# Kernel optimization log

Measured on AMD Instinct MI355X. Metric: run time of the kernel, lower is better.

Reference implementation:

```python
import jax, jax.numpy as jnp
import numpy as np


def setup_inputs() -> dict:
    key = jax.random.key(0)
    kq, kk, kv, kl = jax.random.split(key, 4)
    B, Nq, Nk, D, Dv = 16, 2048, 2048, 128, 128
    queries = jax.random.normal(kq, (B, Nq, D), dtype=jnp.float32)
    keys = jax.random.normal(kk, (B, Nk, D), dtype=jnp.float32)
    values = jax.random.normal(kv, (B, Nk, Dv), dtype=jnp.float32)
    valid_lens = jax.random.randint(kl, (B,), 0, 2048, dtype=jnp.int64)
    return {"queries": queries, "keys": keys, "values": values, "valid_lens": valid_lens}


def reference(queries, keys, values, valid_lens):
    # queries: (B, Nq, d), keys: (B, Nk, d), values: (B, Nk, dv), valid_lens: (B,)
    d = queries.shape[-1]
    scores = jnp.einsum('bqd,bkd->bqk', queries, keys) / jnp.sqrt(jnp.asarray(d, queries.dtype))
    # masked_softmax: original sets masked score positions to 1e-8 (NOT -inf) before softmax
    nk = scores.shape[-1]
    mask = jnp.arange(nk)[None, :] < valid_lens[:, None]  # (B, Nk)
    scores = jnp.where(mask[:, None, :], scores, jnp.asarray(1e-8, scores.dtype))
    attn = jax.nn.softmax(scores, axis=-1)
    # dropout rate 0.0 -> identity (eval semantics)
    return jnp.einsum('bqk,bkv->bqv', attn, values)
```

## Files before the change

### kernel.cpp

```cpp
#include <hip/hip_runtime.h>
#include <stdint.h>

#define BATCH 16
#define NQ    2048
#define NK    2048
#define DD    128
#define DVV   128

typedef __bf16 bf16_t;
typedef __bf16 bf16x2 __attribute__((ext_vector_type(2)));
typedef __bf16 bf16x4 __attribute__((ext_vector_type(4)));
typedef __bf16 bf16x8 __attribute__((ext_vector_type(8)));
typedef float  f32x4  __attribute__((ext_vector_type(4)));

#define KB_OFF   ((size_t)0)
#define VT_OFF   ((size_t)8 * 1024 * 1024)
#define SUF_OFF  ((size_t)16 * 1024 * 1024)
#define SCH_OFF  (SUF_OFF + 65536)
#define WS_NEED  (SCH_OFF + 4096)

__device__ __forceinline__ int load_valid_len(const int* VL, int b) {
  bool looks64 = true;
#pragma unroll
  for (int i = 0; i < 16; ++i) {
    int hi = VL[2 * i + 1];
    unsigned lo = (unsigned)VL[2 * i];
    looks64 = looks64 && (hi == 0) && (lo <= 2048u);
  }
  int L = looks64 ? VL[2 * b] : VL[b];
  return min(max(L, 0), NK);
}

__device__ __forceinline__ void gld16(const void* g, void* l) {
  __builtin_amdgcn_global_load_lds(
      (const __attribute__((address_space(1))) unsigned int*)g,
      (__attribute__((address_space(3))) unsigned int*)l, 16, 0, 0);
}

__device__ __forceinline__ f32x4 mfma16(bf16x8 a, bf16x8 b, f32x4 c) {
  return __builtin_amdgcn_mfma_f32_16x16x32_bf16(a, b, c, 0, 0, 0);
}

__global__ void prep_kernel(const float* __restrict__ K, const float* __restrict__ V,
                            const int* __restrict__ VL,
                            bf16_t* __restrict__ Kb, bf16_t* __restrict__ Vt,
                            float* __restrict__ sufV, int* __restrict__ sched) {
  __shared__ bf16_t tile2[64 * 136];
  __shared__ float sred[16 * 128];
  __shared__ int bs[16];
  const int bid = blockIdx.x;
  const int t = threadIdx.x;
  if (bid < 512) {
#pragma unroll
    for (int i = 0; i < 4; ++i) {
      size_t f4 = (size_t)bid * 2048 + (size_t)i * 512 + 2 * t;
      float4 a = ((const float4*)K)[f4];
      float4 c = ((const float4*)K)[f4 + 1];
      bf16x8 o;
      o[0] = (bf16_t)a.x; o[1] = (bf16_t)a.y; o[2] = (bf16_t)a.z; o[3] = (bf16_t)a.w;
      o[4] = (bf16_t)c.x; o[5] = (bf16_t)c.y; o[6] = (bf16_t)c.z; o[7] = (bf16_t)c.w;
      ((bf16x8*)Kb)[f4 >> 1] = o;
    }
    return;
  }
  if (bid < 1024) {
    int v = bid - 512;
    int b = v & 15, kt = v >> 4;
    int L = load_valid_len(VL, b);
    const bool anymask = (kt * 64 + 64 > L);

    float sacc[8];
#pragma unroll
    for (int j = 0; j < 8; ++j) sacc[j] = 0.f;
    const int c0 = (t & 15) * 8;
#pragma unroll
    for (int i = 0; i < 4; ++i) {
      int rl = i * 16 + (t >> 4);
      const float* src = V + ((size_t)b * NK + kt * 64 + rl) * DVV + c0;
      float4 u0 = ((const float4*)src)[0];
      float4 u1 = ((const float4*)src)[1];
      bf16x8 o;
      o[0] = (bf16_t)u0.x; o[1] = (bf16_t)u0.y; o[2] = (bf16_t)u0.z; o[3] = (bf16_t)u0.w;
      o[4] = (bf16_t)u1.x; o[5] = (bf16_t)u1.y; o[6] = (bf16_t)u1.z; o[7] = (bf16_t)u1.w;
      *(bf16x8*)&tile2[rl * 136 + c0] = o;
      if (kt * 64 + rl >= L) {
        sacc[0] += u0.x; sacc[1] += u0.y; sacc[2] += u0.z; sacc[3] += u0.w;
        sacc[4] += u1.x; sacc[5] += u1.y; sacc[6] += u1.z; sacc[7] += u1.w;
      }
    }
    __syncthreads();

    if (anymask) {
#pragma unroll
      for (int j = 0; j < 8; ++j) sred[(t >> 4) * 128 + c0 + j] = sacc[j];
      __syncthreads();
      if (t < 128) {
        float s = 0.f;
#pragma unroll
        for (int g = 0; g < 16; ++g) s += sred[g * 128 + t];
        atomicAdd(&sufV[b * 128 + t], s);
      }
    }

    int dv = t >> 1, half = t & 1;
    bf16_t* dst = Vt + (size_t)b * DVV * NK + (size_t)dv * NK + kt * 64 + half * 32;
#pragma unroll
    for (int jj = 0; jj < 4; ++jj) {
      bf16x8 o;
#pragma unroll
      for (int k8 = 0; k8 < 8; ++k8)
        o[k8] = tile2[(half * 32 + jj * 8 + k8) * 136 + dv];
      *(bf16x8*)(dst + jj * 8) = o;
    }
    return;
  }
  if (t == 0) {
    int Ls[16], idx[16];
#pragma unroll
    for (int i = 0; i < 16; ++i) { Ls[i] = load_valid_len(VL, i); idx[i] = i; }
    for (int i = 1; i < 16; ++i) {
      int lv = Ls[i], iv = idx[i], j = i - 1;
      while (j >= 0 && Ls[j] < lv) { Ls[j + 1] = Ls[j]; idx[j + 1] = idx[j]; --j; }
      Ls[j + 1] = lv; idx[j + 1] = iv;
    }
#pragma unroll
    for (int i = 0; i < 16; ++i) bs[i] = idx[i];
  }
  __syncthreads();
  for (int j = t; j < 512; j += 256) {
    int r = (j < 256) ? j : (767 - j);
    sched[j] = (bs[r >> 5] << 5) | (r & 31);
  }
}

__launch_bounds__(256, 2)
__global__ void attn_kernel(const float* __restrict__ Q, const bf16_t* __restrict__ Kb,
                            const bf16_t* __restrict__ Vt, const int* __restrict__ VL,
                            const float* __restrict__ sufV, const int* __restrict__ sched,
                            float* __restrict__ Out) {
  __shared__ __align__(16) char smem[73984];
  bf16_t* sK = (bf16_t*)smem;
  bf16_t* sV = (bf16_t*)(smem + 32768);

  const int unit = sched[blockIdx.x];
  const int b  = (unit >> 5) & 15;
  const int qt = unit & 31;
  const int L  = load_valid_len(VL, b);
  const int ktiles = (L + 63) >> 6;

  const int tid = threadIdx.x;
  const int wave = tid >> 6;
  const int lane = tid & 63;
  const int col = lane & 15;
  const int quad = lane >> 4;
  const int wr = wave >> 1;
  const int wc = wave & 1;

  bf16_t* pw = (bf16_t*)(smem + 65536 + wave * 2048);

  bf16x8 qf[2][4];
  {
    const float scq = 0.1275174307f;
#pragma unroll
    for (int m = 0; m < 2; ++m) {
      const float* qrow = Q + ((size_t)b * NQ + qt * 64 + wr * 32 + m * 16 + col) * DD + quad * 8;
#pragma unroll
      for (int ks = 0; ks < 4; ++ks) {
        float4 u0 = *(const float4*)(qrow + ks * 32);
        float4 u1 = *(const float4*)(qrow + ks * 32 + 4);
        bf16x8 f;
        f[0] = (bf16_t)(u0.x * scq); f[1] = (bf16_t)(u0.y * scq);
        f[2] = (bf16_t)(u0.z * scq); f[3] = (bf16_t)(u0.w * scq);
        f[4] = (bf16_t)(u1.x * scq); f[5] = (bf16_t)(u1.y * scq);
        f[6] = (bf16_t)(u1.z * scq); f[7] = (bf16_t)(u1.w * scq);
        qf[m][ks] = f;
      }
    }
  }

  const char* Kbyte = (const char*)Kb + (size_t)b * NK * DD * 2;
  const char* Vbyte = (const char*)Vt + (size_t)b * DVV * NK * 2;
  int koff[4], voff[4];
#pragma unroll
  for (int i = 0; i < 4; ++i) {
    int krow = wave * 16 + i * 4 + (lane >> 4);
    koff[i] = krow * 256 + (((lane & 15) ^ (krow & 15)) * 16);
    int vrow = wave * 32 + i * 8 + (lane >> 3);
    voff[i] = vrow * (NK * 2) + (((lane & 7) ^ ((lane >> 3) & 7)) * 16);
  }

  f32x4 Oacc[2][8];
#pragma unroll
  for (int m = 0; m < 2; ++m)
#pragma unroll
    for (int o = 0; o < 8; ++o) Oacc[m][o] = (f32x4){0.f, 0.f, 0.f, 0.f};
  float lsum[2] = {0.f, 0.f};

  auto issueTile = [&](int kt, int bufi) {
    const char* kb = Kbyte + (size_t)kt * 16384;
    const char* vb = Vbyte + (size_t)kt * 128;
    bf16_t* kl = sK + bufi * 8192 + wave * 2048;
    bf16_t* vl = sV + bufi * 8192 + wave * 2048;
#pragma unroll
    for (int i = 0; i < 4; ++i) {
      gld16(kb + koff[i], kl + i * 512);
      gld16(vb + voff[i], vl + i * 512);
    }
  };

  if (ktiles > 0) issueTile(0, 0);
  int bufi = 0;
  for (int kt = 0; kt < ktiles; ++kt) {
    asm volatile("s_waitcnt vmcnt(0)\n\ts_barrier" ::: "memory");
    if (kt + 1 < ktiles) issueTile(kt + 1, bufi ^ 1);

    const bf16_t* kb_ = sK + bufi * 8192;
    const bf16_t* vb_ = sV + bufi * 8192;

    f32x4 sc[2][2];
#pragma unroll
    for (int ntk = 0; ntk < 2; ++ntk)
#pragma unroll
      for (int m = 0; m < 2; ++m) sc[ntk][m] = (f32x4){0.f, 0.f, 0.f, 0.f};
    __builtin_amdgcn_s_setprio(1);
#pragma unroll
    for (int ks = 0; ks < 4; ++ks) {
#pragma unroll
      for (int ntk = 0; ntk < 2; ++ntk) {
        bf16x8 kf = *(const bf16x8*)&kb_[(wc * 32 + ntk * 16 + col) * 128 + (((ks * 4 + quad) ^ col) * 8)];
        sc[ntk][0] = mfma16(kf, qf[0][ks], sc[ntk][0]);
        sc[ntk][1] = mfma16(kf, qf[1][ks], sc[ntk][1]);
      }
    }
    __builtin_amdgcn_s_setprio(0);

    const int kbase = kt * 64 + wc * 32;
#pragma unroll
    for (int ntk = 0; ntk < 2; ++ntk) {
#pragma unroll
      for (int m = 0; m < 2; ++m) {
        float pv[4];
#pragma unroll
        for (int r = 0; r < 4; ++r) {
          float p = __builtin_amdgcn_exp2f(sc[ntk][m][r]);
          p = (kbase + ntk * 16 + quad * 4 + r < L) ? p : 0.f;
          lsum[m] += p;
          pv[r] = p;
        }
        int cidx = m * 4 + ntk * 2 + (quad >> 1);
        int phys = cidx ^ (col & 7);
        *(bf16x4*)&pw[col * 64 + phys * 8 + (quad & 1) * 4] =
            (bf16x4){(bf16_t)pv[0], (bf16_t)pv[1], (bf16_t)pv[2], (bf16_t)pv[3]};
      }
    }

    bf16x8 pa[2];
#pragma unroll
    for (int m = 0; m < 2; ++m)
      pa[m] = *(const bf16x8*)&pw[col * 64 + (((m * 4 + quad) ^ (col & 7)) * 8)];
    __builtin_amdgcn_s_setprio(1);
#pragma unroll
    for (int o = 0; o < 8; ++o) {
      bf16x8 bb = *(const bf16x8*)&vb_[(o * 16 + col) * 64 + (((wc * 4 + quad) ^ (col & 7)) * 8)];
      Oacc[0][o] = mfma16(pa[0], bb, Oacc[0][o]);
      Oacc[1][o] = mfma16(pa[1], bb, Oacc[1][o]);
    }
    __builtin_amdgcn_s_setprio(0);
    bufi ^= 1;
  }
  __syncthreads();

#pragma unroll
  for (int m = 0; m < 2; ++m) {
    lsum[m] += __shfl_xor(lsum[m], 16, 64);
    lsum[m] += __shfl_xor(lsum[m], 32, 64);
  }

  float* scrO = (float*)(smem + wr * 18432);
  float* scrL = (float*)(smem + 73728) + wr * 32;

  if (wc == 1) {
#pragma unroll
    for (int m = 0; m < 2; ++m)
#pragma unroll
      for (int o = 0; o < 8; ++o)
        *(f32x4*)&scrO[(o * 16 + col) * 36 + m * 16 + quad * 4] = Oacc[m][o];
    if (quad == 0) {
#pragma unroll
      for (int m = 0; m < 2; ++m) scrL[m * 16 + col] = lsum[m];
    }
  }
  __syncthreads();
  if (wc == 0) {
    const float wmask = (float)(NK - L);
    float inv[2];
#pragma unroll
    for (int m = 0; m < 2; ++m)
      inv[m] = 1.0f / (lsum[m] + scrL[m * 16 + col] + wmask);
    float invq[2][4];
#pragma unroll
    for (int m = 0; m < 2; ++m)
#pragma unroll
      for (int r = 0; r < 4; ++r)
        invq[m][r] = __shfl(inv[m], quad * 4 + r, 64);
    const float* sfv = sufV + b * DVV;
    float* Ob = Out + ((size_t)b * NQ + qt * 64 + wr * 32) * DVV;
#pragma unroll
    for (int m = 0; m < 2; ++m)
#pragma unroll
      for (int o = 0; o < 8; ++o) {
        f32x4 part = *(const f32x4*)&scrO[(o * 16 + col) * 36 + m * 16 + quad * 4];
        float svv = sfv[o * 16 + col];
#pragma unroll
        for (int r = 0; r < 4; ++r)
          Ob[(size_t)(m * 16 + quad * 4 + r) * DVV + o * 16 + col] =
              (Oacc[m][o][r] + part[r] + svv) * invq[m][r];
      }
  }
}

#define KSTR 152
#define VSTR 88
#define PSTR 72

__global__ void suffix_fb(const float* __restrict__ V, const int* __restrict__ VL,
                          float* __restrict__ ws) {
  int b = blockIdx.x;
  int kc = blockIdx.y;
  int L = load_valid_len(VL, b);
  int k0 = kc * 128, k1 = k0 + 128;
  int lo = max(L, k0);
  int t = threadIdx.x;
  int dv = t & 127;
  int h = t >> 7;
  float s = 0.f;
  for (int k = lo + h; k < k1; k += 2)
    s += V[((size_t)b * NK + k) * DVV + dv];
  __shared__ float part[128];
  if (h == 0) part[dv] = s;
  __syncthreads();
  if (h == 1) atomicAdd(&ws[b * DVV + dv], part[dv] + s);
}

__launch_bounds__(256, 2)
__global__ void attn_fb(const float* __restrict__ Q, const float* __restrict__ K,
                        const float* __restrict__ V, const int* __restrict__ VL,
                        const float* __restrict__ sufV, float* __restrict__ Out) {
  const int flat = blockIdx.x;
  const int b  = flat & 15;
  const int qt = flat >> 4;
  const int L  = load_valid_len(VL, b);

  __shared__ bf16_t sK2[64 * KSTR];
  __shared__ bf16_t sVT2[128 * VSTR];
  __shared__ bf16_t sP2[4 * 16 * PSTR];

  const int tid  = threadIdx.x;
  const int wave = tid >> 6;
  const int lane = tid & 63;
  const int col  = lane & 15;
  const int quad = lane >> 4;

  const float* Qb = Q + ((size_t)b * NQ + qt * 64 + wave * 16) * DD;
  const float* Kb = K + (size_t)b * NK * DD;
  const float* Vb = V + (size_t)b * NK * DVV;

  bf16x8 qf[4];
  {
    const float scq = 0.08838834764831845f;
    const float* qrow = Qb + (size_t)col * DD + quad * 8;
#pragma unroll
    for (int ks = 0; ks < 4; ++ks) {
      float4 u0 = *(const float4*)(qrow + ks * 32);
      float4 u1 = *(const float4*)(qrow + ks * 32 + 4);
      bf16x8 f;
      f[0] = (bf16_t)(u0.x * scq); f[1] = (bf16_t)(u0.y * scq);
      f[2] = (bf16_t)(u0.z * scq); f[3] = (bf16_t)(u0.w * scq);
      f[4] = (bf16_t)(u1.x * scq); f[5] = (bf16_t)(u1.y * scq);
      f[6] = (bf16_t)(u1.z * scq); f[7] = (bf16_t)(u1.w * scq);
      qf[ks] = f;
    }
  }

  f32x4 Oacc[8];
#pragma unroll
  for (int o = 0; o < 8; ++o) Oacc[o] = (f32x4){0.f, 0.f, 0.f, 0.f};
  float m_i[4], l_i[4];
#pragma unroll
  for (int r = 0; r < 4; ++r) { m_i[r] = -1e30f; l_i[r] = 0.f; }

  const int ktiles = (L + 63) >> 6;
  for (int kt = 0; kt < ktiles; ++kt) {
    {
      int r0 = tid >> 5;
      int d4 = (tid & 31) * 4;
      const float* src = Kb + ((size_t)(kt * 64) + r0) * DD + d4;
#pragma unroll
      for (int i = 0; i < 8; ++i) {
        float4 u = *(const float4*)(src + (size_t)i * 8 * DD);
        bf16x4 w4 = {(bf16_t)u.x, (bf16_t)u.y, (bf16_t)u.z, (bf16_t)u.w};
        *(bf16x4*)&sK2[(r0 + i * 8) * KSTR + d4] = w4;
      }
    }
    {
      int r2 = (tid & 31) * 2;
      int dbase = (tid >> 5) * 4;
#pragma unroll
      for (int i = 0; i < 4; ++i) {
        int d4 = dbase + i * 32;
        const float* s0 = Vb + ((size_t)(kt * 64) + r2) * DVV + d4;
        float4 u0 = *(const float4*)s0;
        float4 u1 = *(const float4*)(s0 + DVV);
        *(bf16x2*)&sVT2[(d4 + 0) * VSTR + r2] = (bf16x2){(bf16_t)u0.x, (bf16_t)u1.x};
        *(bf16x2*)&sVT2[(d4 + 1) * VSTR + r2] = (bf16x2){(bf16_t)u0.y, (bf16_t)u1.y};
        *(bf16x2*)&sVT2[(d4 + 2) * VSTR + r2] = (bf16x2){(bf16_t)u0.z, (bf16_t)u1.z};
        *(bf16x2*)&sVT2[(d4 + 3) * VSTR + r2] = (bf16x2){(bf16_t)u0.w, (bf16_t)u1.w};
      }
    }
    __syncthreads();

    f32x4 sv4[4];
#pragma unroll
    for (int nt = 0; nt < 4; ++nt) sv4[nt] = (f32x4){0.f, 0.f, 0.f, 0.f};
#pragma unroll
    for (int ks = 0; ks < 4; ++ks) {
      bf16x8 a = qf[ks];
#pragma unroll
      for (int nt = 0; nt < 4; ++nt) {
        bf16x8 bb = *(const bf16x8*)&sK2[(nt * 16 + col) * KSTR + ks * 32 + quad * 8];
        sv4[nt] = mfma16(a, bb, sv4[nt]);
      }
    }

    const int key0 = kt * 64;
    float sv[4][4];
    float mloc[4] = {-1e30f, -1e30f, -1e30f, -1e30f};
#pragma unroll
    for (int nt = 0; nt < 4; ++nt) {
      int key = key0 + nt * 16 + col;
      bool valid = key < L;
#pragma unroll
      for (int r = 0; r < 4; ++r) {
        float v = valid ? sv4[nt][r] : -1e30f;
        sv[nt][r] = v;
        mloc[r] = fmaxf(mloc[r], v);
      }
    }
#pragma unroll
    for (int off = 1; off < 16; off <<= 1)
#pragma unroll
      for (int r = 0; r < 4; ++r) mloc[r] = fmaxf(mloc[r], __shfl_xor(mloc[r], off, 64));
    float al[4];
#pragma unroll
    for (int r = 0; r < 4; ++r) {
      float mn = fmaxf(m_i[r], mloc[r]);
      al[r] = __expf(m_i[r] - mn);
      m_i[r] = mn;
    }
    float lloc[4] = {0.f, 0.f, 0.f, 0.f};
#pragma unroll
    for (int nt = 0; nt < 4; ++nt)
#pragma unroll
      for (int r = 0; r < 4; ++r) {
        float p = __expf(sv[nt][r] - m_i[r]);
        sv[nt][r] = p;
        lloc[r] += p;
      }
#pragma unroll
    for (int off = 1; off < 16; off <<= 1)
#pragma unroll
      for (int r = 0; r < 4; ++r) lloc[r] += __shfl_xor(lloc[r], off, 64);
#pragma unroll
    for (int r = 0; r < 4; ++r) l_i[r] = l_i[r] * al[r] + lloc[r];
#pragma unroll
    for (int o = 0; o < 8; ++o)
#pragma unroll
      for (int r = 0; r < 4; ++r) Oacc[o][r] *= al[r];

    bf16_t* pw = &sP2[wave * 16 * PSTR];
#pragma unroll
    for (int nt = 0; nt < 4; ++nt)
#pragma unroll
      for (int r = 0; r < 4; ++r)
        pw[(quad * 4 + r) * PSTR + nt * 16 + col] = (bf16_t)sv[nt][r];

#pragma unroll
    for (int ks2 = 0; ks2 < 2; ++ks2) {
      bf16x8 a = *(const bf16x8*)&pw[(lane & 15) * PSTR + ks2 * 32 + quad * 8];
#pragma unroll
      for (int o = 0; o < 8; ++o) {
        bf16x8 bb = *(const bf16x8*)&sVT2[(o * 16 + col) * VSTR + ks2 * 32 + quad * 8];
        Oacc[o] = mfma16(a, bb, Oacc[o]);
      }
    }
    __syncthreads();
  }

  if (L < NK) {
    const float c = 1e-8f;
    const float w = (float)(NK - L);
    float a2[4], ec[4];
#pragma unroll
    for (int r = 0; r < 4; ++r) {
      float mn = fmaxf(m_i[r], c);
      a2[r] = __expf(m_i[r] - mn);
      ec[r] = __expf(c - mn);
      l_i[r] = l_i[r] * a2[r] + w * ec[r];
    }
    const float* sfv = sufV + b * DVV;
#pragma unroll
    for (int o = 0; o < 8; ++o) {
      float svv = sfv[o * 16 + col];
#pragma unroll
      for (int r = 0; r < 4; ++r) Oacc[o][r] = Oacc[o][r] * a2[r] + ec[r] * svv;
    }
  }

  float invl[4];
#pragma unroll
  for (int r = 0; r < 4; ++r) invl[r] = 1.0f / l_i[r];

  float* Ob = Out + ((size_t)b * NQ + qt * 64 + wave * 16) * DVV;
#pragma unroll
  for (int o = 0; o < 8; ++o)
#pragma unroll
    for (int r = 0; r < 4; ++r)
      Ob[(size_t)(quad * 4 + r) * DVV + o * 16 + col] = Oacc[o][r] * invl[r];
}

extern "C" void kernel_launch(void* const* d_in, const int* in_sizes, int n_in,
                              void* d_out, int out_size, void* d_ws, size_t ws_size,
                              hipStream_t stream) {
  const float* Q  = (const float*)d_in[0];
  const float* K  = (const float*)d_in[1];
  const float* V  = (const float*)d_in[2];
  const int*   VL = (const int*)d_in[3];
  float* out = (float*)d_out;

  if (ws_size >= WS_NEED) {
    char* ws = (char*)d_ws;
    bf16_t* Kb = (bf16_t*)(ws + KB_OFF);
    bf16_t* Vt = (bf16_t*)(ws + VT_OFF);
    float* sufV = (float*)(ws + SUF_OFF);
    int* sched = (int*)(ws + SCH_OFF);

    hipMemsetAsync(sufV, 0, BATCH * DVV * sizeof(float), stream);
    prep_kernel<<<1025, 256, 0, stream>>>(K, V, VL, Kb, Vt, sufV, sched);
    attn_kernel<<<512, 256, 0, stream>>>(Q, Kb, Vt, VL, sufV, sched, out);
  } else {
    float* ws = (float*)d_ws;
    hipMemsetAsync(ws, 0, BATCH * DVV * sizeof(float), stream);
    dim3 g1(BATCH, 16);
    suffix_fb<<<g1, 256, 0, stream>>>(V, VL, ws);
    attn_fb<<<BATCH * (NQ / 64), 256, 0, stream>>>(Q, K, V, VL, ws, out);
  }
}
```

Measured before the change: 141.9 us.

## Drop memset and schedule table; fuse K/V prep blocks, reduce suffix partials in attention

The hipMemsetAsync and the atomic suffix accumulation are removed. Each prep block now writes a per-tile partial masked-value sum, which the attention kernel reduces in its epilogue. The K-conversion and V-transpose blocks are merged into one 512-block prep kernel, and each attention block now computes the length-sorted schedule itself instead of reading a precomputed table. This saves a launch and the atomics, at the cost of a small redundant sort and 32 extra partial-sum loads per attention block.

```diff
diff --git a/kernel.cpp b/kernel.cpp
--- a/kernel.cpp
+++ b/kernel.cpp
@@ -15,9 +15,8 @@
 
 #define KB_OFF   ((size_t)0)
 #define VT_OFF   ((size_t)8 * 1024 * 1024)
-#define SUF_OFF  ((size_t)16 * 1024 * 1024)
-#define SCH_OFF  (SUF_OFF + 65536)
-#define WS_NEED  (SCH_OFF + 4096)
+#define PSUF_OFF ((size_t)16 * 1024 * 1024)
+#define WS_NEED  (PSUF_OFF + 262144)
 
 __device__ __forceinline__ int load_valid_len(const int* VL, int b) {
   bool looks64 = true;
@@ -41,114 +40,97 @@
   return __builtin_amdgcn_mfma_f32_16x16x32_bf16(a, b, c, 0, 0, 0);
 }
 
-__global__ void prep_kernel(const float* __restrict__ K, const float* __restrict__ V,
-                            const int* __restrict__ VL,
-                            bf16_t* __restrict__ Kb, bf16_t* __restrict__ Vt,
-                            float* __restrict__ sufV, int* __restrict__ sched) {
+__global__ void prep2_kernel(const float* __restrict__ Kf, const float* __restrict__ Vf,
+                             const int* __restrict__ VL,
+                             bf16_t* __restrict__ Kb, bf16_t* __restrict__ Vt,
+                             float* __restrict__ partSuf) {
   __shared__ bf16_t tile2[64 * 136];
   __shared__ float sred[16 * 128];
-  __shared__ int bs[16];
-  const int bid = blockIdx.x;
+  const int g = blockIdx.x;
   const int t = threadIdx.x;
-  if (bid < 512) {
-#pragma unroll
-    for (int i = 0; i < 4; ++i) {
-      size_t f4 = (size_t)bid * 2048 + (size_t)i * 512 + 2 * t;
-      float4 a = ((const float4*)K)[f4];
-      float4 c = ((const float4*)K)[f4 + 1];
-      bf16x8 o;
-      o[0] = (bf16_t)a.x; o[1] = (bf16_t)a.y; o[2] = (bf16_t)a.z; o[3] = (bf16_t)a.w;
-      o[4] = (bf16_t)c.x; o[5] = (bf16_t)c.y; o[6] = (bf16_t)c.z; o[7] = (bf16_t)c.w;
-      ((bf16x8*)Kb)[f4 >> 1] = o;
-    }
-    return;
-  }
-  if (bid < 1024) {
-    int v = bid - 512;
-    int b = v & 15, kt = v >> 4;
-    int L = load_valid_len(VL, b);
-    const bool anymask = (kt * 64 + 64 > L);
-
-    float sacc[8];
-#pragma unroll
-    for (int j = 0; j < 8; ++j) sacc[j] = 0.f;
-    const int c0 = (t & 15) * 8;
-#pragma unroll
-    for (int i = 0; i < 4; ++i) {
-      int rl = i * 16 + (t >> 4);
-      const float* src = V + ((size_t)b * NK + kt * 64 + rl) * DVV + c0;
-      float4 u0 = ((const float4*)src)[0];
-      float4 u1 = ((const float4*)src)[1];
-      bf16x8 o;
-      o[0] = (bf16_t)u0.x; o[1] = (bf16_t)u0.y; o[2] = (bf16_t)u0.z; o[3] = (bf16_t)u0.w;
-      o[4] = (bf16_t)u1.x; o[5] = (bf16_t)u1.y; o[6] = (bf16_t)u1.z; o[7] = (bf16_t)u1.w;
-      *(bf16x8*)&tile2[rl * 136 + c0] = o;
-      if (kt * 64 + rl >= L) {
-        sacc[0] += u0.x; sacc[1] += u0.y; sacc[2] += u0.z; sacc[3] += u0.w;
-        sacc[4] += u1.x; sacc[5] += u1.y; sacc[6] += u1.z; sacc[7] += u1.w;
-      }
-    }
-    __syncthreads();
-
-    if (anymask) {
-#pragma unroll
-      for (int j = 0; j < 8; ++j) sred[(t >> 4) * 128 + c0 + j] = sacc[j];
-      __syncthreads();
-      if (t < 128) {
-        float s = 0.f;
-#pragma unroll
-        for (int g = 0; g < 16; ++g) s += sred[g * 128 + t];
-        atomicAdd(&sufV[b * 128 + t], s);
-      }
-    }
-
-    int dv = t >> 1, half = t & 1;
-    bf16_t* dst = Vt + (size_t)b * DVV * NK + (size_t)dv * NK + kt * 64 + half * 32;
-#pragma unroll
-    for (int jj = 0; jj < 4; ++jj) {
-      bf16x8 o;
-#pragma unroll
-      for (int k8 = 0; k8 < 8; ++k8)
-        o[k8] = tile2[(half * 32 + jj * 8 + k8) * 136 + dv];
-      *(bf16x8*)(dst + jj * 8) = o;
-    }
-    return;
-  }
-  if (t == 0) {
-    int Ls[16], idx[16];
-#pragma unroll
-    for (int i = 0; i < 16; ++i) { Ls[i] = load_valid_len(VL, i); idx[i] = i; }
-    for (int i = 1; i < 16; ++i) {
-      int lv = Ls[i], iv = idx[i], j = i - 1;
-      while (j >= 0 && Ls[j] < lv) { Ls[j + 1] = Ls[j]; idx[j + 1] = idx[j]; --j; }
-      Ls[j + 1] = lv; idx[j + 1] = iv;
-    }
-#pragma unroll
-    for (int i = 0; i < 16; ++i) bs[i] = idx[i];
+
+#pragma unroll
+  for (int i = 0; i < 4; ++i) {
+    size_t f4 = (size_t)g * 2048 + (size_t)i * 512 + 2 * t;
+    float4 a = ((const float4*)Kf)[f4];
+    float4 c = ((const float4*)Kf)[f4 + 1];
+    bf16x8 o;
+    o[0] = (bf16_t)a.x; o[1] = (bf16_t)a.y; o[2] = (bf16_t)a.z; o[3] = (bf16_t)a.w;
+    o[4] = (bf16_t)c.x; o[5] = (bf16_t)c.y; o[6] = (bf16_t)c.z; o[7] = (bf16_t)c.w;
+    ((bf16x8*)Kb)[f4 >> 1] = o;
+  }
+
+  int b = g & 15, kt = g >> 4;
+  int L = load_valid_len(VL, b);
+  float sacc[8];
+#pragma unroll
+  for (int j = 0; j < 8; ++j) sacc[j] = 0.f;
+  const int c0 = (t & 15) * 8;
+#pragma unroll
+  for (int i = 0; i < 4; ++i) {
+    int rl = i * 16 + (t >> 4);
+    const float* src = Vf + ((size_t)b * NK + kt * 64 + rl) * DVV + c0;
+    float4 u0 = ((const float4*)src)[0];
+    float4 u1 = ((const float4*)src)[1];
+    bf16x8 o;
+    o[0] = (bf16_t)u0.x; o[1] = (bf16_t)u0.y; o[2] = (bf16_t)u0.z; o[3] = (bf16_t)u0.w;
+    o[4] = (bf16_t)u1.x; o[5] = (bf16_t)u1.y; o[6] = (bf16_t)u1.z; o[7] = (bf16_t)u1.w;
+    *(bf16x8*)&tile2[rl * 136 + c0] = o;
+    if (kt * 64 + rl >= L) {
+      sacc[0] += u0.x; sacc[1] += u0.y; sacc[2] += u0.z; sacc[3] += u0.w;
+      sacc[4] += u1.x; sacc[5] += u1.y; sacc[6] += u1.z; sacc[7] += u1.w;
+    }
   }
   __syncthreads();
-  for (int j = t; j < 512; j += 256) {
-    int r = (j < 256) ? j : (767 - j);
-    sched[j] = (bs[r >> 5] << 5) | (r & 31);
+#pragma unroll
+  for (int j = 0; j < 8; ++j) sred[(t >> 4) * 128 + c0 + j] = sacc[j];
+  __syncthreads();
+  if (t < 128) {
+    float s = 0.f;
+#pragma unroll
+    for (int gg = 0; gg < 16; ++gg) s += sred[gg * 128 + t];
+    partSuf[(size_t)g * 128 + t] = s;
+  }
+  int dv = t >> 1, half = t & 1;
+  bf16_t* dst = Vt + (size_t)b * DVV * NK + (size_t)dv * NK + kt * 64 + half * 32;
+#pragma unroll
+  for (int jj = 0; jj < 4; ++jj) {
+    bf16x8 o;
+#pragma unroll
+    for (int k8 = 0; k8 < 8; ++k8)
+      o[k8] = tile2[(half * 32 + jj * 8 + k8) * 136 + dv];
+    *(bf16x8*)(dst + jj * 8) = o;
   }
 }
 
 __launch_bounds__(256, 2)
 __global__ void attn_kernel(const float* __restrict__ Q, const bf16_t* __restrict__ Kb,
                             const bf16_t* __restrict__ Vt, const int* __restrict__ VL,
-                            const float* __restrict__ sufV, const int* __restrict__ sched,
-                            float* __restrict__ Out) {
+                            const float* __restrict__ partSuf, float* __restrict__ Out) {
   __shared__ __align__(16) char smem[73984];
   bf16_t* sK = (bf16_t*)smem;
   bf16_t* sV = (bf16_t*)(smem + 32768);
 
-  const int unit = sched[blockIdx.x];
+  const int tid = threadIdx.x;
+  int unit;
+  {
+    int Ls[16], idx[16];
+#pragma unroll
+    for (int i = 0; i < 16; ++i) { Ls[i] = load_valid_len(VL, i); idx[i] = i; }
+    for (int i = 1; i < 16; ++i) {
+      int lv = Ls[i], iv = idx[i], jj = i - 1;
+      while (jj >= 0 && Ls[jj] < lv) { Ls[jj + 1] = Ls[jj]; idx[jj + 1] = idx[jj]; --jj; }
+      Ls[jj + 1] = lv; idx[jj + 1] = iv;
+    }
+    int gg = blockIdx.x;
+    int r = (gg < 256) ? gg : (767 - gg);
+    unit = (idx[r >> 5] << 5) | (r & 31);
+  }
   const int b  = (unit >> 5) & 15;
   const int qt = unit & 31;
   const int L  = load_valid_len(VL, b);
   const int ktiles = (L + 63) >> 6;
 
-  const int tid = threadIdx.x;
   const int wave = tid >> 6;
   const int lane = tid & 63;
   const int col = lane & 15;
@@ -270,6 +252,16 @@
   }
   __syncthreads();
 
+  float* sred2 = (float*)(smem + 36864);
+  {
+    int dv = tid & 127, h = tid >> 7;
+    float part = 0.f;
+#pragma unroll
+    for (int j = 0; j < 16; ++j)
+      part += partSuf[(size_t)((h * 16 + j) * 16 + b) * 128 + dv];
+    sred2[tid] = part;
+  }
+
 #pragma unroll
   for (int m = 0; m < 2; ++m) {
     lsum[m] += __shfl_xor(lsum[m], 16, 64);
@@ -303,14 +295,13 @@
 #pragma unroll
       for (int r = 0; r < 4; ++r)
         invq[m][r] = __shfl(inv[m], quad * 4 + r, 64);
-    const float* sfv = sufV + b * DVV;
     float* Ob = Out + ((size_t)b * NQ + qt * 64 + wr * 32) * DVV;
 #pragma unroll
     for (int m = 0; m < 2; ++m)
 #pragma unroll
       for (int o = 0; o < 8; ++o) {
         f32x4 part = *(const f32x4*)&scrO[(o * 16 + col) * 36 + m * 16 + quad * 4];
-        float svv = sfv[o * 16 + col];
+        float svv = sred2[o * 16 + col] + sred2[128 + o * 16 + col];
 #pragma unroll
         for (int r = 0; r < 4; ++r)
           Ob[(size_t)(m * 16 + quad * 4 + r) * DVV + o * 16 + col] =
@@ -541,12 +532,10 @@
     char* ws = (char*)d_ws;
     bf16_t* Kb = (bf16_t*)(ws + KB_OFF);
     bf16_t* Vt = (bf16_t*)(ws + VT_OFF);
-    float* sufV = (float*)(ws + SUF_OFF);
-    int* sched = (int*)(ws + SCH_OFF);
-
-    hipMemsetAsync(sufV, 0, BATCH * DVV * sizeof(float), stream);
-    prep_kernel<<<1025, 256, 0, stream>>>(K, V, VL, Kb, Vt, sufV, sched);
-    attn_kernel<<<512, 256, 0, stream>>>(Q, Kb, Vt, VL, sufV, sched, out);
+    float* psuf = (float*)(ws + PSUF_OFF);
+
+    prep2_kernel<<<512, 256, 0, stream>>>(K, V, VL, Kb, Vt, psuf);
+    attn_kernel<<<512, 256, 0, stream>>>(Q, Kb, Vt, VL, psuf, out);
   } else {
     float* ws = (float*)d_ws;
     hipMemsetAsync(ws, 0, BATCH * DVV * sizeof(float), stream);
```

After: 151.2 us. 1.07x slower.
